# Optimization experiments

Measured on AMD Instinct MI355X. Metric: run time of the kernel, lower is better.

The kernel has to match this reference:

```python
import jax, jax.numpy as jnp
import numpy as np

B = 2
C = 256
NA = 3  # aspect ratios per location
IMG_H, IMG_W = 800, 1216
FEAT_SHAPES = [(200, 304), (100, 152), (50, 76), (25, 38), (13, 19)]
STRIDES = [4, 8, 16, 32, 64]
SIZES = [32, 64, 128, 256, 512]
RATIOS = np.array([0.5, 1.0, 2.0])
PRE_NMS = 1000
POST_NMS = 1000
NMS_TH = 0.7
MIN_SIZE = 1e-3
BBOX_CLIP = float(np.log(1000.0 / 16.0))
NUM_PER_LEVEL = [h * w * NA for h, w in FEAT_SHAPES]


def _make_anchors():
    out = []
    for (h, w), stride, size in zip(FEAT_SHAPES, STRIDES, SIZES):
        hr = np.sqrt(RATIOS)
        wr = 1.0 / hr
        ws, hs = wr * size, hr * size
        base = np.stack([-ws / 2, -hs / 2, ws / 2, hs / 2], 1)  # [NA,4]
        yy, xx = np.meshgrid(np.arange(h) * stride, np.arange(w) * stride, indexing='ij')
        shifts = np.stack([xx.ravel(), yy.ravel(), xx.ravel(), yy.ravel()], 1)  # [h*w,4]
        out.append((shifts[:, None, :] + base[None, :, :]).reshape(-1, 4))
    return jnp.asarray(np.concatenate(out, 0), jnp.float32)  # [A,4]

ANCHORS = _make_anchors()
# level id of each selected (per-level top-k) anchor is static
LEVELS_SEL = jnp.asarray(
    np.concatenate([np.full(min(PRE_NMS, a), i) for i, a in enumerate(NUM_PER_LEVEL)]),
    jnp.float32)


def conv2d(x, w, b, pad):
    y = jax.lax.conv_general_dilated(x, w, (1, 1), [(pad, pad), (pad, pad)],
                                     dimension_numbers=('NCHW', 'OIHW', 'NCHW'))
    return y + b[None, :, None, None]


def decode(reg, anc):
    # BoxCoder.decode with weights (1,1,1,1)
    wa = anc[..., 2] - anc[..., 0]
    ha = anc[..., 3] - anc[..., 1]
    cxa = anc[..., 0] + 0.5 * wa
    cya = anc[..., 1] + 0.5 * ha
    dx, dy = reg[..., 0], reg[..., 1]
    dw = jnp.minimum(reg[..., 2], BBOX_CLIP)
    dh = jnp.minimum(reg[..., 3], BBOX_CLIP)
    cx = dx * wa + cxa
    cy = dy * ha + cya
    w = jnp.exp(dw) * wa
    h = jnp.exp(dh) * ha
    return jnp.stack([cx - 0.5 * w, cy - 0.5 * h, cx + 0.5 * w, cy + 0.5 * h], -1)


def _nms_select(boxes, scores, valid, lvl_offsets):
    # batched_nms via per-level coordinate offset trick; greedy NMS over IoU matrix
    b = boxes + lvl_offsets[:, None]
    s = jnp.where(valid, scores, -jnp.inf)
    order = jnp.argsort(-s)
    bs = b[order]
    keep = valid[order]
    area = (bs[:, 2] - bs[:, 0]) * (bs[:, 3] - bs[:, 1])
    lt = jnp.maximum(bs[:, None, :2], bs[None, :, :2])
    rb = jnp.minimum(bs[:, None, 2:], bs[None, :, 2:])
    wh = jnp.clip(rb - lt, 0.0)
    inter = wh[..., 0] * wh[..., 1]
    iou = inter / (area[:, None] + area[None, :] - inter + 1e-9)
    K = boxes.shape[0]
    ar = jnp.arange(K)

    def body(i, keep):
        sup = keep[i] & (iou[i] > NMS_TH) & (ar > i)
        return keep & ~sup

    keep = jax.lax.fori_loop(0, K, body, keep)
    keep_orig = jnp.zeros(K, bool).at[order].set(keep)
    ms = jnp.where(keep_orig, scores, -jnp.inf)
    top_s, idx = jax.lax.top_k(ms, POST_NMS)
    return idx, jnp.isfinite(top_s)


def reference(feat0, feat1, feat2, feat3, feat4, conv_w, conv_b, cls_w, cls_b, box_w, box_b):
    logit_l, reg_l = [], []
    for f in (feat0, feat1, feat2, feat3, feat4):
        t = jax.nn.relu(conv2d(f, conv_w, conv_b, 1))
        l = conv2d(t, cls_w, cls_b, 0)   # [B,NA,H,W]
        r = conv2d(t, box_w, box_b, 0)   # [B,NA*4,H,W]
        _, _, H, W = l.shape
        logit_l.append(l.transpose(0, 2, 3, 1).reshape(B, -1))                        # HWC order
        reg_l.append(r.reshape(B, NA, 4, H, W).transpose(0, 3, 4, 1, 2).reshape(B, -1, 4))
    logits = jnp.concatenate(logit_l, 1)   # [B,A]
    regs = jnp.concatenate(reg_l, 1)       # [B,A,4]
    proposals = decode(regs, ANCHORS[None])  # [B,A,4]

    # per-level top-k (pre-NMS)
    sel, off = [], 0
    for a in NUM_PER_LEVEL:
        k = min(PRE_NMS, a)
        _, idx = jax.lax.top_k(logits[:, off:off + a], k)
        sel.append(idx + off)
        off += a
    sel = jnp.concatenate(sel, 1)          # [B,Ksel]
    bi = jnp.arange(B)[:, None]
    sc = logits[bi, sel]
    bx = proposals[bi, sel]

    # clip to image, remove small boxes (mask)
    x0 = jnp.clip(bx[..., 0], 0.0, float(IMG_W))
    y0 = jnp.clip(bx[..., 1], 0.0, float(IMG_H))
    x1 = jnp.clip(bx[..., 2], 0.0, float(IMG_W))
    y1 = jnp.clip(bx[..., 3], 0.0, float(IMG_H))
    bx = jnp.stack([x0, y0, x1, y1], -1)
    valid = ((x1 - x0) >= MIN_SIZE) & ((y1 - y0) >= MIN_SIZE)
    offs = LEVELS_SEL * (float(max(IMG_W, IMG_H)) + 1.0)

    idx2, vout = jax.vmap(lambda b_, s_, v_: _nms_select(b_, s_, v_, offs))(
        jax.lax.stop_gradient(bx), jax.lax.stop_gradient(sc), valid)

    boxes_out = jnp.take_along_axis(bx, idx2[..., None], 1)   # [B,POST_NMS,4]
    scores_out = jnp.take_along_axis(sc, idx2, 1)             # [B,POST_NMS]
    boxes_out = jnp.where(vout[..., None], boxes_out, 0.0)
    scores_out = jnp.where(vout, scores_out, -1e9)
    return boxes_out, scores_out


def setup_inputs() -> dict:
    key = jax.random.key(0)
    ks = jax.random.split(key, 9)
    inp = {}
    for i, (h, w) in enumerate(FEAT_SHAPES):
        inp[f'feat{i}'] = jax.random.normal(ks[i], (B, C, h, w), jnp.float32)
    inp['conv_w'] = jax.random.normal(ks[5], (C, C, 3, 3), jnp.float32) * 0.01
    inp['conv_b'] = jnp.zeros((C,), jnp.float32)
    inp['cls_w'] = jax.random.normal(ks[6], (NA, C, 1, 1), jnp.float32) * 0.01
    inp['cls_b'] = jnp.zeros((NA,), jnp.float32)
    inp['box_w'] = jax.random.normal(ks[7], (NA * 4, C, 1, 1), jnp.float32) * 0.01
    inp['box_b'] = jnp.zeros((NA * 4,), jnp.float32)
    return inp
```

## Files before the change

### kernel.cpp

```cpp
#include <hip/hip_runtime.h>
#include <hip/hip_fp16.h>
#include <stdint.h>
#include <math.h>

typedef unsigned int uint;
typedef unsigned short ushort;
typedef unsigned long long ull;
typedef __attribute__((ext_vector_type(8))) _Float16 f16x8;
typedef __attribute__((ext_vector_type(4))) float f32x4;

#define BATCH 2
#define ATOTAL 242991
#define KSEL 4741
#define NW 75
#define POST_NMS 1000
#define WB_ELEMS (2*8*3*3*2*8*64*8)
#define NPAIRS 2850

__device__ __constant__ int dLoff[5]  = {0,182400,228000,239400,242250};
__device__ __constant__ int dCount[5] = {182400,45600,11400,2850,741};
__device__ __constant__ int dSeg[5]   = {0,1000,2000,3000,4000};
__device__ __constant__ int dSegK[5]  = {1000,1000,1000,1000,741};
__device__ __constant__ int dHc[5]     = {200,100,50,25,13};
__device__ __constant__ int dWc[5]     = {304,152,76,38,19};
__device__ __constant__ int dTilesX[5] = {19,10,5,3,2};
__device__ __constant__ int dCumT[6]   = {0,475,605,640,652,656};
__device__ __constant__ int dStrideC[5]= {4,8,16,32,64};
__device__ __constant__ int dSizeC[5]  = {32,64,128,256,512};

__device__ __forceinline__ uint fkey(float f) {
    uint u = __float_as_uint(f);
    return (u & 0x80000000u) ? ~u : (u | 0x80000000u);
}
__device__ __forceinline__ ushort h2u(__half h) {
    union { __half h; ushort u; } x; x.h = h; return x.u;
}

__global__ __launch_bounds__(256) void wt_kernel(const float* __restrict__ conv_w,
                                                 ushort* __restrict__ wB) {
    int t = blockIdx.x * 256 + threadIdx.x;
    if (t >= WB_ELEMS) return;
    int e    = t & 7;
    int lane = (t >> 3) & 63;
    int nt   = (t >> 9) & 7;
    int pl   = (t >> 12) & 1;
    int r    = t >> 13;
    int dx = r % 3; r /= 3;
    int dy = r % 3; r /= 3;
    int icblk = r & 7;
    int ocg = r >> 3;
    int oc = ocg * 128 + nt * 16 + (lane & 15);
    int ic = icblk * 32 + ((lane >> 4) << 3) + e;
    float v = conv_w[(size_t)oc * 2304 + ic * 9 + dy * 3 + dx];
    __half h = __float2half(v);
    float rr = (v - __half2float(h)) * 1024.0f;
    __half m = __float2half(rr);
    wB[t] = (pl == 0) ? h2u(h) : h2u(m);
}

__global__ __launch_bounds__(512) void conv_mfma_all(
    const float* __restrict__ f0, const float* __restrict__ f1,
    const float* __restrict__ f2, const float* __restrict__ f3,
    const float* __restrict__ f4, const ushort* __restrict__ wB,
    const float* __restrict__ conv_b,
    const float* __restrict__ cls_w, const float* __restrict__ cls_b,
    const float* __restrict__ box_w, const float* __restrict__ box_b,
    float* __restrict__ scoresA, float* __restrict__ boxesA)
{
    const int bidx = blockIdx.x;
    const int b    = blockIdx.y;
    const int tid  = threadIdx.x;

    int lvl = 0;
#pragma unroll
    for (int l = 1; l < 5; ++l) if (bidx >= dCumT[l]) lvl = l;
    const int tile   = bidx - dCumT[lvl];
    const int H      = dHc[lvl], W = dWc[lvl];
    const int TILESX = dTilesX[lvl];
    const int ty0    = (tile / TILESX) * 8;
    const int tx0    = (tile % TILESX) * 16;
    const int HW     = H * W;
    const float* feat = (lvl == 0) ? f0 : (lvl == 1) ? f1 : (lvl == 2) ? f2 : (lvl == 3) ? f3 : f4;
    const float* fb = feat + (size_t)b * 256 * HW;

    __shared__ __align__(16) char uni[72192];
    ushort* halo = (ushort*)uni;
    ushort* ldsB = (ushort*)(uni + 23040);
    float*  tS   = (float*)uni;
    float*  hw2  = (float*)(uni + 32768);
    double* houtD= (double*)uni;

    const int lane = tid & 63, wave = tid >> 6;
    const int wm = wave >> 1, wn = wave & 1;
    const int g = lane >> 4, col = lane & 15;
    const int laneA = g * 1440 + col * 8;

    int  hdst[12]; int hoff[12]; bool hval[12];
#pragma unroll
    for (int j = 0; j < 12; ++j) {
        int e = tid + j * 512;
        hdst[j] = -1; hoff[j] = 0; hval[j] = false;
        if (e < 5760) {
            int ic = e / 180, rem = e - ic * 180;
            int hrow = rem / 18, hcol = rem - hrow * 18;
            int gy = ty0 + hrow - 1, gx = tx0 + hcol - 1;
            hdst[j] = (((ic >> 3) * 10 + hrow) * 18 + hcol) * 8 + (ic & 7);
            if (gy >= 0 && gy < H && gx >= 0 && gx < W) {
                hval[j] = true; hoff[j] = ic * HW + gy * W + gx;
            }
        }
    }

    double hacc[4] = {0,0,0,0};

    uint4 Br0, Br1, Br2, Br3, Br4, Br5;
    {
        const uint4* gq = (const uint4*)wB;
        Br0 = gq[tid];        Br1 = gq[tid + 512];
        Br2 = gq[tid + 1024]; Br3 = gq[tid + 1536];
        Br4 = gq[tid + 2048]; Br5 = gq[tid + 2560];
    }

#pragma unroll 1
    for (int ocg = 0; ocg < 2; ++ocg) {
        f32x4 accH[2][4], accM[2][4];
#pragma unroll
        for (int mi = 0; mi < 2; ++mi)
#pragma unroll
            for (int ni = 0; ni < 4; ++ni) {
                accH[mi][ni] = (f32x4){0.f, 0.f, 0.f, 0.f};
                accM[mi][ni] = (f32x4){0.f, 0.f, 0.f, 0.f};
            }

#pragma unroll 1
        for (int s = 0; s < 24; ++s) {
            const int icblk = s / 3;
            const int dy    = s - icblk * 3;

            __syncthreads();
            if (dy == 0) {
                float hv[12];
                const float* fcb = fb + (size_t)icblk * 32 * HW;
#pragma unroll
                for (int j = 0; j < 12; ++j)
                    hv[j] = hval[j] ? fcb[hoff[j]] : 0.f;
#pragma unroll
                for (int j = 0; j < 12; ++j) {
                    if (hdst[j] >= 0) {
                        float v = hv[j];
                        __half h = __float2half(v);
                        float rr = (v - __half2float(h)) * 1024.0f;
                        __half m = __float2half(rr);
                        int li = hdst[j];
                        halo[li] = h2u(h); halo[5760 + li] = h2u(m);
                    }
                }
            }
            {
                uint4* lq = (uint4*)ldsB;
                lq[tid] = Br0;         lq[tid + 512]  = Br1;
                lq[tid + 1024] = Br2;  lq[tid + 1536] = Br3;
                lq[tid + 2048] = Br4;  lq[tid + 2560] = Br5;
            }
            __syncthreads();
            {
                int gstep = ocg * 24 + s + 1;
                if (gstep < 48) {
                    const uint4* gq = (const uint4*)(wB + (size_t)gstep * 24576);
                    Br0 = gq[tid];        Br1 = gq[tid + 512];
                    Br2 = gq[tid + 1024]; Br3 = gq[tid + 1536];
                    Br4 = gq[tid + 2048]; Br5 = gq[tid + 2560];
                }
            }
#pragma unroll 1
            for (int dx = 0; dx < 3; ++dx) {
                f16x8 Ah[2], Am[2];
                const int abase = laneA + dx * 8 + (2 * wm + dy) * 144;
#pragma unroll
                for (int mi = 0; mi < 2; ++mi) {
                    Ah[mi] = *(const f16x8*)(halo + abase + mi * 144);
                    Am[mi] = *(const f16x8*)(halo + 5760 + abase + mi * 144);
                }
#pragma unroll
                for (int ni = 0; ni < 4; ++ni) {
                    const int nt = 4 * wn + ni;
                    f16x8 Bh = *(const f16x8*)(ldsB + (size_t)(dx * 16 + nt) * 512 + lane * 8);
                    f16x8 Bm = *(const f16x8*)(ldsB + (size_t)(dx * 16 + 8 + nt) * 512 + lane * 8);
#pragma unroll
                    for (int mi = 0; mi < 2; ++mi) {
                        f32x4 cH = accH[mi][ni];
                        f32x4 cM = accM[mi][ni];
                        cH = __builtin_amdgcn_mfma_f32_16x16x32_f16(Ah[mi], Bh, cH, 0, 0, 0);
                        cM = __builtin_amdgcn_mfma_f32_16x16x32_f16(Ah[mi], Bm, cM, 0, 0, 0);
                        cM = __builtin_amdgcn_mfma_f32_16x16x32_f16(Am[mi], Bh, cM, 0, 0, 0);
                        accH[mi][ni] = cH;
                        accM[mi][ni] = cM;
                    }
                }
            }
        }
        __syncthreads();
        float cb[4];
#pragma unroll
        for (int ni = 0; ni < 4; ++ni)
            cb[ni] = conv_b[ocg * 128 + (4 * wn + ni) * 16 + col];

#pragma unroll 1
        for (int s2 = 0; s2 < 2; ++s2) {
            if (wn == s2) {
#pragma unroll
                for (int mi = 0; mi < 2; ++mi) {
#pragma unroll
                    for (int r = 0; r < 4; ++r) {
                        int px = (2 * wm + mi) * 16 + 4 * g + r;
                        int sw = px & 15;
#pragma unroll
                        for (int ni = 0; ni < 4; ++ni) {
                            int slot = (ni * 4 + (col >> 2)) ^ sw;
                            float val = accH[mi][ni][r] + accM[mi][ni][r] * 0.0009765625f;
                            tS[px * 64 + slot * 4 + (col & 3)] =
                                fmaxf(val + cb[ni], 0.f);
                        }
                    }
                }
            }
            if (tid < 256) {
                const int oc2 = tid >> 2;
                const int h0  = (tid & 3) * 4;
                const int oc  = ocg * 128 + s2 * 64 + oc2;
                float vv[4];
#pragma unroll
                for (int q = 0; q < 4; ++q) {
                    int h = h0 + q;
                    vv[q] = (h < 3) ? cls_w[h * 256 + oc]
                          : (h < 15) ? box_w[(h - 3) * 256 + oc] : 0.f;
                }
                *(float4*)&hw2[oc2 * 16 + h0] = make_float4(vv[0], vv[1], vv[2], vv[3]);
            }
            __syncthreads();
            {
                const int px = tid & 127;
                const int hh = tid >> 7;
                const int sw = px & 15;
#pragma unroll 1
                for (int j4 = 0; j4 < 16; ++j4) {
                    float4 t4 = *(const float4*)&tS[px * 64 + (j4 ^ sw) * 4];
                    float tv[4] = {t4.x, t4.y, t4.z, t4.w};
#pragma unroll
                    for (int jj = 0; jj < 4; ++jj) {
                        const float* hb = &hw2[(j4 * 4 + jj) * 16 + hh * 4];
                        float4 h0 = *(const float4*)hb;
                        double tv_d = (double)tv[jj];
                        hacc[0] += tv_d * (double)h0.x;
                        hacc[1] += tv_d * (double)h0.y;
                        hacc[2] += tv_d * (double)h0.z;
                        hacc[3] += tv_d * (double)h0.w;
                    }
                }
            }
            __syncthreads();
        }
    }

    {
        const int px = tid & 127;
        const int hh = tid >> 7;
#pragma unroll
        for (int j = 0; j < 4; ++j) houtD[px * 16 + hh * 4 + j] = hacc[j];
    }
    __syncthreads();

    if (tid < 128) {
        const int px = tid;
        const int gy = ty0 + (px >> 4);
        const int gx = tx0 + (px & 15);
        if (gy < H && gx < W) {
            const int STRIDE = dStrideC[lvl];
            const int SZ     = dSizeC[lvl];
            const int LOFF   = dLoff[lvl];
#pragma unroll 1
            for (int a = 0; a < 3; ++a) {
                double score = houtD[px * 16 + a] + (double)cls_b[a];
                double rg0 = houtD[px * 16 + 3 + a * 4 + 0] + (double)box_b[a * 4 + 0];
                double rg1 = houtD[px * 16 + 3 + a * 4 + 1] + (double)box_b[a * 4 + 1];
                double rg2 = houtD[px * 16 + 3 + a * 4 + 2] + (double)box_b[a * 4 + 2];
                double rg3 = houtD[px * 16 + 3 + a * 4 + 3] + (double)box_b[a * 4 + 3];
                double ratio = (a == 0) ? 0.5 : ((a == 1) ? 1.0 : 2.0);
                double hr = sqrt(ratio), wr = 1.0 / hr;
                double wsd = wr * (double)SZ, hsd = hr * (double)SZ;
                double sx = (double)(gx * STRIDE), sy = (double)(gy * STRIDE);
                float ax0 = (float)(sx - 0.5 * wsd);
                float ay0 = (float)(sy - 0.5 * hsd);
                float ax1 = (float)(sx + 0.5 * wsd);
                float ay1 = (float)(sy + 0.5 * hsd);
                double wa = (double)ax1 - (double)ax0, ha = (double)ay1 - (double)ay0;
                double cxa = (double)ax0 + 0.5 * wa, cya = (double)ay0 + 0.5 * ha;
                double dwv = fmin(rg2, 4.135166556742356);
                double dhv = fmin(rg3, 4.135166556742356);
                double cx = rg0 * wa + cxa, cy = rg1 * ha + cya;
                double w = exp(dwv) * wa, h = exp(dhv) * ha;
                double x0 = cx - 0.5 * w, y0 = cy - 0.5 * h;
                double x1 = cx + 0.5 * w, y1 = cy + 0.5 * h;
                x0 = fmin(fmax(x0, 0.0), 1216.0);
                y0 = fmin(fmax(y0, 0.0), 800.0);
                x1 = fmin(fmax(x1, 0.0), 1216.0);
                y1 = fmin(fmax(y1, 0.0), 800.0);
                int gidx = LOFF + (gy * W + gx) * 3 + a;
                scoresA[(size_t)b * ATOTAL + gidx] = (float)score;
                float4 bx = make_float4((float)x0, (float)y0, (float)x1, (float)y1);
                *(float4*)&boxesA[((size_t)b * ATOTAL + gidx) * 4] = bx;
            }
        }
    }
}

__global__ __launch_bounds__(1024) void topk_kernel(
    const float* __restrict__ scoresA, const float* __restrict__ boxesA,
    float* __restrict__ selScore, float* __restrict__ selBox,
    int* __restrict__ selValid, int* __restrict__ selAnchor)
{
    const int lvl = blockIdx.x, b = blockIdx.y;
    const int n = dCount[lvl], loff = dLoff[lvl], seg = dSeg[lvl], k = dSegK[lvl];
    const float* sc = scoresA + (size_t)b * ATOTAL + loff;
    const int tid = threadIdx.x;

    float* oS = selScore + b * KSEL;
    float* oB = selBox + (size_t)b * KSEL * 4;
    int* oV = selValid + b * KSEL;
    int* oA = selAnchor + b * KSEL;

    auto emit = [&](int slot, int i) {
        int g = loff + i;
        float s = sc[i];
        float4 bx = *(const float4*)&boxesA[((size_t)b * ATOTAL + g) * 4];
        oS[seg + slot] = s;
        *(float4*)&oB[(size_t)(seg + slot) * 4] = bx;
        oV[seg + slot] = ((bx.z - bx.x) >= 1e-3f && (bx.w - bx.y) >= 1e-3f) ? 1 : 0;
        oA[seg + slot] = g;
    };

    if (n <= k) {
        for (int i = tid; i < n; i += 1024) emit(i, i);
        return;
    }

    __shared__ uint hist[2048];
    __shared__ uint sh_bin, sh_krem;
    __shared__ uint cntG, cntE;
    __shared__ int stash[64];

    uint krem = (uint)k;
    uint prefix = 0;
    for (int pass = 0; pass < 3; ++pass) {
        for (int e = tid; e < 2048; e += 1024) hist[e] = 0;
        __syncthreads();
        for (int i = tid; i < n; i += 1024) {
            uint key = fkey(sc[i]);
            uint bin; bool sel;
            if (pass == 0)      { sel = true;                      bin = key >> 21; }
            else if (pass == 1) { sel = ((key >> 21) == prefix);   bin = (key >> 10) & 0x7FFu; }
            else                { sel = ((key >> 10) == prefix);   bin = key & 0x3FFu; }
            if (sel) atomicAdd(&hist[bin], 1u);
        }
        __syncthreads();
        if (tid == 0) {
            int nb = (pass == 2) ? 1024 : 2048;
            uint c = 0;
            for (int x = nb - 1; x >= 0; --x) {
                uint h = hist[x];
                if (c + h >= krem) { sh_bin = (uint)x; sh_krem = krem - c; break; }
                c += h;
            }
        }
        __syncthreads();
        uint bin = sh_bin; krem = sh_krem;
        if (pass == 0)      prefix = bin;
        else if (pass == 1) prefix = (prefix << 11) | bin;
        else                prefix = (prefix << 10) | bin;
        __syncthreads();
    }
    const uint T = prefix;
    const uint need_eq = krem;
    if (tid == 0) { cntG = 0; cntE = 0; }
    __syncthreads();
    for (int i = tid; i < n; i += 1024) {
        uint key = fkey(sc[i]);
        if (key > T) {
            uint pos = atomicAdd(&cntG, 1u);
            emit((int)pos, i);
        } else if (key == T) {
            uint e = atomicAdd(&cntE, 1u);
            if (e < 64) stash[e] = i;
        }
    }
    __syncthreads();
    if (tid == 0) {
        uint ne = cntE < 64u ? cntE : 64u;
        uint base = cntG;
        for (uint t2 = 0; t2 < need_eq; ++t2) {
            int best = -1, bj = -1;
            for (uint j2 = 0; j2 < ne; ++j2) {
                int v = stash[j2];
                if (v >= 0 && (best < 0 || v < best)) { best = v; bj = j2; }
            }
            if (bj >= 0) { stash[bj] = -1; emit((int)(base + t2), best); }
            else emit((int)(base + t2), 0);
        }
    }
}

__global__ __launch_bounds__(1024) void sort_kernel(
    const float* __restrict__ selScore, const float* __restrict__ selBox,
    const int* __restrict__ selValid, const int* __restrict__ selAnchor,
    int* __restrict__ sortedSlot, float* __restrict__ sortedBoxOff,
    ull* __restrict__ validMask)
{
    const int b = blockIdx.x, tid = threadIdx.x;
    __shared__ ull  skey[8192];
    __shared__ uint spay[8192];
    __shared__ ull  svm[NW];

    for (int i = tid; i < 8192; i += 1024) {
        ull kk2; uint pp;
        if (i < KSEL) {
            float s = selScore[b * KSEL + i];
            int v = selValid[b * KSEL + i];
            uint k32 = v ? fkey(s) : 0x007FFFFFu;
            uint a32 = 0xFFFFFFFFu - (uint)selAnchor[b * KSEL + i];
            kk2 = ((ull)k32 << 32) | a32; pp = (uint)i;
        } else { kk2 = 0ull; pp = 0xFFFFFFFFu; }
        skey[i] = kk2; spay[i] = pp;
    }
    __syncthreads();
    for (uint kk = 2; kk <= 8192; kk <<= 1) {
        for (uint j = kk >> 1; j > 0; j >>= 1) {
            for (int i = tid; i < 8192; i += 1024) {
                uint ixj = (uint)i ^ j;
                if (ixj > (uint)i) {
                    bool up = ((((uint)i) & kk) == 0);
                    ull a = skey[i], c = skey[ixj];
                    bool sw = up ? (a < c) : (a > c);
                    if (sw) {
                        skey[i] = c; skey[ixj] = a;
                        uint tp = spay[i]; spay[i] = spay[ixj]; spay[ixj] = tp;
                    }
                }
            }
            __syncthreads();
        }
    }
    for (int i = tid; i < NW; i += 1024) svm[i] = 0ull;
    __syncthreads();
    for (int i = tid; i < KSEL; i += 1024) {
        uint slot = spay[i];
        sortedSlot[b * KSEL + i] = (int)slot;
        int v = selValid[b * KSEL + slot];
        if (v) atomicOr(&svm[i >> 6], 1ull << (i & 63));
        int lvl = (int)slot / 1000;
        float off = 1217.0f * (float)lvl;
        float4 bx = *(const float4*)&selBox[((size_t)b * KSEL + slot) * 4];
        bx.x += off; bx.y += off; bx.z += off; bx.w += off;
        *(float4*)&sortedBoxOff[((size_t)b * KSEL + i) * 4] = bx;
    }
    __syncthreads();
    for (int i = tid; i < NW; i += 1024) validMask[b * NW + i] = svm[i];
}

__global__ __launch_bounds__(64) void nms_mask(const float* __restrict__ sortedBoxOff,
                                               ull* __restrict__ mat)
{
    const int b = blockIdx.y;
    const int tid = threadIdx.x;
    int rem = blockIdx.x, ib = 0;
    while (rem >= NW - ib) { rem -= NW - ib; ++ib; }
    const int jb = ib + rem;

    __shared__ float4 bj[64];
    __shared__ float  aj[64];
    const int j0 = jb * 64;
    const int jn = (KSEL - j0) < 64 ? (KSEL - j0) : 64;
    if (tid < jn) {
        float4 v = *(const float4*)&sortedBoxOff[((size_t)b * KSEL + j0 + tid) * 4];
        bj[tid] = v; aj[tid] = (v.z - v.x) * (v.w - v.y);
    }
    __syncthreads();
    const int i = ib * 64 + tid;
    if (i >= KSEL) return;
    float4 bi = *(const float4*)&sortedBoxOff[((size_t)b * KSEL + i) * 4];
    float ai = (bi.z - bi.x) * (bi.w - bi.y);
    ull m = 0ull;
    for (int jj = 0; jj < jn; ++jj) {
        int j = j0 + jj;
        if (j <= i) continue;
        float4 bb = bj[jj];
        float ltx = fmaxf(bi.x, bb.x), lty = fmaxf(bi.y, bb.y);
        float rbx = fminf(bi.z, bb.z), rby = fminf(bi.w, bb.w);
        float wx = fmaxf(rbx - ltx, 0.f), wy = fmaxf(rby - lty, 0.f);
        float inter = wx * wy;
        float iou = inter / (ai + aj[jj] - inter + 1e-9f);
        if (iou > 0.7f) m |= (1ull << jj);
    }
    mat[((size_t)b * KSEL + i) * NW + jb] = m;
}

#define LOADG(RA, RB, G) { int base0 = (G) * 16; \
    _Pragma("unroll") for (int d = 0; d < 16; ++d) { int i = base0 + d; \
        RA[d] = (i < KSEL) ? mb[(size_t)i * NW + lane] : 0ull; \
        RB[d] = (hasHi && i < KSEL) ? mb[(size_t)i * NW + 64 + lane] : 0ull; } }
#define PROCG(RA, RB, G) { int base0 = (G) * 16; \
    _Pragma("unroll") for (int d = 0; d < 16; ++d) { int i = base0 + d; \
        if (i < KSEL) { int wi = i >> 6; \
            ull act0 = v0 & ~s0, act1 = v1 & ~s1; \
            ull aw = (wi < 64) ? __shfl(act0, wi, 64) : __shfl(act1, wi - 64, 64); \
            if ((aw >> (i & 63)) & 1ull) { \
                s0 |= (lane >= wi) ? RA[d] : 0ull; \
                s1 |= (lane + 64 >= wi) ? RB[d] : 0ull; \
                if (lane == 0) keptPos[b * POST_NMS + nk] = i; \
                ++nk; \
                if (nk == POST_NMS) { if (lane == 0) nkOut[b] = nk; return; } } } } }

__global__ __launch_bounds__(64) void nms_scan(const ull* __restrict__ mat,
                                               const ull* __restrict__ validMask,
                                               int* __restrict__ keptPos,
                                               int* __restrict__ nkOut)
{
    const int b = blockIdx.x, lane = threadIdx.x;
    const bool hasHi = lane < NW - 64;
    ull v0 = validMask[b * NW + lane];
    ull v1 = hasHi ? validMask[b * NW + 64 + lane] : 0ull;
    ull s0 = 0ull, s1 = 0ull;
    int nk = 0;
    const ull* mb = mat + (size_t)b * KSEL * NW;
    const int NG = (KSEL + 15) / 16;

    ull A0[16], B0[16], A1[16], B1[16];
    LOADG(A0, B0, 0);
    for (int g = 0; g < NG; g += 2) {
        if (g + 1 < NG) LOADG(A1, B1, g + 1);
        PROCG(A0, B0, g);
        if (g + 2 < NG) LOADG(A0, B0, g + 2);
        if (g + 1 < NG) PROCG(A1, B1, g + 1);
    }
    if (lane == 0) nkOut[b] = nk;
}

__global__ __launch_bounds__(256) void out_kernel(
    const int* __restrict__ keptPos, const int* __restrict__ nkOut,
    const int* __restrict__ sortedSlot,
    const float* __restrict__ selBox, const float* __restrict__ selScore,
    float* __restrict__ out)
{
    int t = blockIdx.x * 256 + threadIdx.x;
    if (t >= BATCH * POST_NMS) return;
    int b = t / POST_NMS, row = t - b * POST_NMS;
    float4 bx = make_float4(0.f, 0.f, 0.f, 0.f);
    float sc = -1e9f;
    if (row < nkOut[b]) {
        int i = keptPos[b * POST_NMS + row];
        int slot = sortedSlot[b * KSEL + i];
        bx = *(const float4*)&selBox[((size_t)b * KSEL + slot) * 4];
        sc = selScore[b * KSEL + slot];
    }
    *(float4*)&out[(size_t)t * 4] = bx;
    out[BATCH * POST_NMS * 4 + t] = sc;
}

extern "C" void kernel_launch(void* const* d_in, const int* in_sizes, int n_in,
                              void* d_out, int out_size, void* d_ws, size_t ws_size,
                              hipStream_t stream)
{
    (void)in_sizes; (void)n_in; (void)out_size; (void)ws_size;
    const float* feat[5] = {(const float*)d_in[0], (const float*)d_in[1],
                            (const float*)d_in[2], (const float*)d_in[3],
                            (const float*)d_in[4]};
    const float* conv_w = (const float*)d_in[5];
    const float* conv_b = (const float*)d_in[6];
    const float* cls_w  = (const float*)d_in[7];
    const float* cls_b  = (const float*)d_in[8];
    const float* box_w  = (const float*)d_in[9];
    const float* box_b  = (const float*)d_in[10];
    float* out = (float*)d_out;

    char* ws = (char*)d_ws;
    size_t off = 0;
    auto carve = [&](size_t bytes) -> void* {
        void* p = (void*)(ws + off);
        off += (bytes + 255) & ~(size_t)255;
        return p;
    };
    ushort* wB         = (ushort*)carve((size_t)WB_ELEMS * 2);
    float* scoresA     = (float*)carve((size_t)BATCH * ATOTAL * 4);
    float* boxesA      = (float*)carve((size_t)BATCH * ATOTAL * 16);
    float* selScore    = (float*)carve((size_t)BATCH * KSEL * 4);
    float* selBox      = (float*)carve((size_t)BATCH * KSEL * 16);
    int*   selValid    = (int*)  carve((size_t)BATCH * KSEL * 4);
    int*   selAnchor   = (int*)  carve((size_t)BATCH * KSEL * 4);
    int*   sortedSlot  = (int*)  carve((size_t)BATCH * KSEL * 4);
    float* sortedBoxOff= (float*)carve((size_t)BATCH * KSEL * 16);
    ull*   validMask   = (ull*)  carve((size_t)BATCH * NW * 8);
    ull*   mat         = (ull*)  carve((size_t)BATCH * KSEL * NW * 8);
    int*   keptPos     = (int*)  carve((size_t)BATCH * POST_NMS * 4);
    int*   nkOut       = (int*)  carve(64);

    wt_kernel<<<(WB_ELEMS + 255) / 256, 256, 0, stream>>>(conv_w, wB);

    conv_mfma_all<<<dim3(656, BATCH), 512, 0, stream>>>(
        feat[0], feat[1], feat[2], feat[3], feat[4], wB, conv_b,
        cls_w, cls_b, box_w, box_b, scoresA, boxesA);

    topk_kernel<<<dim3(5, BATCH), 1024, 0, stream>>>(scoresA, boxesA, selScore, selBox, selValid, selAnchor);
    sort_kernel<<<dim3(BATCH), 1024, 0, stream>>>(selScore, selBox, selValid, selAnchor, sortedSlot, sortedBoxOff, validMask);
    nms_mask<<<dim3(NPAIRS, BATCH), 64, 0, stream>>>(sortedBoxOff, mat);
    nms_scan<<<dim3(BATCH), 64, 0, stream>>>(mat, validMask, keptPos, nkOut);
    out_kernel<<<dim3((BATCH * POST_NMS + 255) / 256), 256, 0, stream>>>(keptPos, nkOut, sortedSlot, selBox, selScore, out);
}
```

Measured before the change: 1.527 ms.

## Parallelize radix-select histogram bin search and raise wave priority around MFMA

Replaces the single-thread serial backward scan over the 2048-bin histogram in the per-level top-k radix select with a block-wide suffix-sum scan. Each of the 1024 threads then checks its own pair of bins for the crossing point. It also wraps the conv MFMA inner block with s_setprio to favor matrix-issuing waves. The scan trades a long serial loop on one thread for about ten block barriers per pass, and needs extra shared memory.

After: 1.479 ms. -3.1%, faster.

```diff
diff --git a/kernel.cpp b/kernel.cpp
--- a/kernel.cpp
+++ b/kernel.cpp
@@ -186,6 +186,7 @@
                     const int nt = 4 * wn + ni;
                     f16x8 Bh = *(const f16x8*)(ldsB + (size_t)(dx * 16 + nt) * 512 + lane * 8);
                     f16x8 Bm = *(const f16x8*)(ldsB + (size_t)(dx * 16 + 8 + nt) * 512 + lane * 8);
+                    __builtin_amdgcn_s_setprio(1);
 #pragma unroll
                     for (int mi = 0; mi < 2; ++mi) {
                         f32x4 cH = accH[mi][ni];
@@ -196,6 +197,7 @@
                         accH[mi][ni] = cH;
                         accM[mi][ni] = cM;
                     }
+                    __builtin_amdgcn_s_setprio(0);
                 }
             }
         }
@@ -345,6 +347,7 @@
     }
 
     __shared__ uint hist[2048];
+    __shared__ uint suf[2][1024];
     __shared__ uint sh_bin, sh_krem;
     __shared__ uint cntG, cntE;
     __shared__ int stash[64];
@@ -363,13 +366,32 @@
             if (sel) atomicAdd(&hist[bin], 1u);
         }
         __syncthreads();
-        if (tid == 0) {
-            int nb = (pass == 2) ? 1024 : 2048;
-            uint c = 0;
-            for (int x = nb - 1; x >= 0; --x) {
-                uint h = hist[x];
-                if (c + h >= krem) { sh_bin = (uint)x; sh_krem = krem - c; break; }
-                c += h;
+        {
+            const int nb = (pass == 2) ? 1024 : 2048;
+            uint pv = 0;
+            if (2 * tid < nb)     pv += hist[2 * tid];
+            if (2 * tid + 1 < nb) pv += hist[2 * tid + 1];
+            suf[0][tid] = pv;
+            __syncthreads();
+            int src = 0;
+#pragma unroll
+            for (int off2 = 1; off2 < 1024; off2 <<= 1) {
+                uint v = suf[src][tid] + ((tid + off2 < 1024) ? suf[src][tid + off2] : 0u);
+                suf[src ^ 1][tid] = v;
+                __syncthreads();
+                src ^= 1;
+            }
+            uint SUFt1 = (tid + 1 < 1024) ? suf[src][tid + 1] : 0u;
+            uint h1 = (2 * tid + 1 < nb) ? hist[2 * tid + 1] : 0u;
+            if (2 * tid + 1 < nb && SUFt1 < krem && SUFt1 + h1 >= krem) {
+                sh_bin = (uint)(2 * tid + 1); sh_krem = krem - SUFt1;
+            }
+            uint S0 = SUFt1 + h1;
+            if (2 * tid < nb) {
+                uint h0 = hist[2 * tid];
+                if (S0 < krem && S0 + h0 >= krem) {
+                    sh_bin = (uint)(2 * tid); sh_krem = krem - S0;
+                }
             }
         }
         __syncthreads();
```
